# Performance work log

Measured on AMD Instinct MI355X. Metric: run time of the kernel, lower is better.

Reference implementation:

```python
import jax, jax.numpy as jnp
import numpy as np

NUM_MAPS = 512
NUM_BLOCKS = 2
ZG = 512
HID = min(96, NUM_MAPS)          # shared query / attention hidden dim
SEQ = 8                           # hardcoded inner sequence length
H1 = min(NUM_MAPS // 32, 3)       # num_heads1 = 3
H2 = NUM_MAPS // 32               # num_heads2 = 16
NPROC = NUM_BLOCKS * 4            # 4 FiLM param types per block


def _mha(q, k, v, nheads):
    """Multi-head attention. q:(Lq,D) k,v:(Lk,D) -> (Lq,D)."""
    Lq, D = q.shape
    Lk = k.shape[0]
    d = D // nheads
    qh = q.reshape(Lq, nheads, d).transpose(1, 0, 2)   # (h,Lq,d)
    kh = k.reshape(Lk, nheads, d).transpose(1, 0, 2)
    vh = v.reshape(Lk, nheads, d).transpose(1, 0, 2)
    A = jax.nn.softmax(jnp.einsum('hqd,hkd->hqk', qh, kh) / jnp.sqrt(jnp.asarray(D, q.dtype)))
    O = jnp.einsum('hqk,hkd->hqd', A, vh)
    return O.transpose(1, 0, 2).reshape(Lq, D)


def setup_inputs() -> dict:
    key = jax.random.key(0)
    ks = jax.random.split(key, 20)
    s = 0.05
    n = jax.random.normal
    return {
        'gate': jax.random.uniform(ks[0], (1, SEQ), dtype=jnp.float32),
        'x': n(ks[1], (1, ZG), dtype=jnp.float32),
        # shared_layer_alphaC : Linear(ZG, NUM_MAPS) + Sigmoid
        'Wa': n(ks[2], (ZG, NUM_MAPS)) * s, 'ba': jnp.zeros((NUM_MAPS,)),
        # shared_layer_Query : Linear(ZG, HID) + ReLU
        'Wqr': n(ks[3], (ZG, HID)) * s, 'bqr': jnp.zeros((HID,)),
        # stacked FiLM params: [block, {g1,b1,g2,b2}, num_maps, 8]
        'P': n(ks[4], (NUM_BLOCKS, 4, NUM_MAPS, SEQ)) * 0.2,
        'De': n(ks[5], (NUM_BLOCKS, 4, NUM_MAPS, SEQ)) * 0.01,
        'regs': n(ks[6], (NUM_BLOCKS, 4, NUM_MAPS)) * 0.001,
        # SMAB_small processor weights, stacked over the 8 processors
        'Wq1': n(ks[7], (NPROC, NUM_MAPS, HID)) * s,
        'Wk1': n(ks[8], (NPROC, NUM_MAPS, HID)) * s,
        'Wv1': n(ks[9], (NPROC, NUM_MAPS, HID)) * s,
        'fc1': n(ks[10], (NPROC, HID, HID)) * s,
        'Wq2': n(ks[11], (NPROC, HID, HID)) * s,
        'Wk2': n(ks[12], (NPROC, HID, HID)) * s,
        'Wv2': n(ks[13], (NPROC, HID, HID)) * s,
        'fc2': n(ks[14], (NPROC, HID, HID)) * s,
        'Wo': n(ks[15], (NPROC, HID, NUM_MAPS)) * s,
    }


def reference(gate, x, Wa, ba, Wqr, bqr, P, De, regs,
              Wq1, Wk1, Wv1, fc1, Wq2, Wk2, Wv2, fc2, Wo):
    alpha = jax.nn.sigmoid(x @ Wa + ba).reshape(-1)        # (NUM_MAPS,)
    q = jax.nn.relu(x @ Wqr + bqr)                          # (1, HID)

    # per-processor key/value set: transpose(1,0).view(1,8,num_maps)
    K_all = P.reshape(NPROC, NUM_MAPS, SEQ).transpose(0, 2, 1)  # (8procs, 8, NUM_MAPS)

    def smab(K, wq1, wk1, wv1, f1, wq2, wk2, wv2, f2, wo):
        # stage 1: self-attention over the 8-element set (num_heads1)
        Qk = K @ wq1                                        # (8, HID)
        H = Qk + _mha(Qk, K @ wk1, K @ wv1, H1)
        H = H + jax.nn.relu(H @ f1)
        # stage 2: task query attends to the set (num_heads2)
        Qq = q @ wq2                                        # (1, HID)
        O = Qq + _mha(Qq, H @ wk2, H @ wv2, H2)
        O = O + jax.nn.relu(O @ f2)
        return (O @ wo)[0]                                  # (NUM_MAPS,)

    trans = jax.vmap(smab)(K_all, Wq1, Wk1, Wv1, fc1, Wq2, Wk2, Wv2, fc2, Wo)
    trans = trans.reshape(NUM_BLOCKS, 4, NUM_MAPS)

    de = (De * gate[0]).sum(-1)                             # (NB,4,NUM_MAPS)
    mix = alpha * trans + (1.0 - alpha) * de
    offs = jnp.array([1.0, 0.0, 1.0, 0.0], dtype=mix.dtype).reshape(1, 4, 1)
    # gamma gets +1 offset, beta does not
    return mix * regs + offs
```

## Files before the change

kernel.cpp:

```cpp
#include <hip/hip_runtime.h>
#include <hip/hip_bf16.h>
#include <math.h>


#define WS_ALPHA 0
#define WS_Q     512
#define WS_QKV   608
#define WS_H     19040
#define WS_QQ    25184
#define WS_H2    25952
#define WS_K2    32096
#define WS_V2    38240
#define WS_OF    44384

__global__ __launch_bounds__(256) void k1_qkv_alpha_q(
    const float* __restrict__ x, const float* __restrict__ Wa,
    const float* __restrict__ ba, const float* __restrict__ Wqr,
    const float* __restrict__ bqr, const float* __restrict__ P,
    const float* __restrict__ Wq1, const float* __restrict__ Wk1,
    const float* __restrict__ Wv1, float* __restrict__ ws)
{
    __shared__ float sK[8 * 512];
    __shared__ float sp[256];
    const int blk = blockIdx.x, tid = threadIdx.x;

    if (blk < 576) {
        const int proc = blk / 72, c = blk % 72;
        const float4* P4 = (const float4*)(P + proc * 4096);
        for (int i = tid; i < 1024; i += 256) {
            float4 v = P4[i];
            const int m = i >> 1, off = (i & 1) * 4;
            sK[(off + 0) * 512 + m] = v.x;
            sK[(off + 1) * 512 + m] = v.y;
            sK[(off + 2) * 512 + m] = v.z;
            sK[(off + 3) * 512 + m] = v.w;
        }
        __syncthreads();
        const int rl = tid & 31, sp8 = tid >> 5;
        const int r = c * 32 + rl;
        const int mat = r / 768, r2 = r % 768;
        const int s = r2 / 96, h = r2 % 96;
        const float* W = (mat == 0 ? Wq1 : (mat == 1 ? Wk1 : Wv1))
                         + proc * 49152 + (sp8 * 64) * 96 + h;
        const float* Ks = sK + s * 512 + sp8 * 64;
        float acc = 0.f;
        #pragma unroll
        for (int m2 = 0; m2 < 64; ++m2) acc += Ks[m2] * W[m2 * 96];
        sp[tid] = acc;
        __syncthreads();
        if (sp8 == 0) {
            float a = 0.f;
            #pragma unroll
            for (int j = 0; j < 8; ++j) a += sp[rl + 32 * j];
            ws[WS_QKV + proc * 2304 + r] = a;
        }
    } else if (blk < 592) {
        for (int k = tid; k < 512; k += 256) sK[k] = x[k];
        __syncthreads();
        const int ml = tid & 31, sp8 = tid >> 5;
        const int m = (blk - 576) * 32 + ml;
        const float* W = Wa + (sp8 * 64) * 512 + m;
        const float* xq = sK + sp8 * 64;
        float acc = 0.f;
        #pragma unroll
        for (int k = 0; k < 64; ++k) acc += xq[k] * W[k * 512];
        sp[tid] = acc;
        __syncthreads();
        if (sp8 == 0) {
            float a = ba[m];
            #pragma unroll
            for (int j = 0; j < 8; ++j) a += sp[ml + 32 * j];
            ws[WS_ALPHA + m] = 1.f / (1.f + __expf(-a));
        }
    } else {
        for (int k = tid; k < 512; k += 256) sK[k] = x[k];
        __syncthreads();
        const int hl = tid & 31, sp8 = tid >> 5;
        const int h = (blk - 592) * 32 + hl;
        const float* W = Wqr + (sp8 * 64) * 96 + h;
        const float* xq = sK + sp8 * 64;
        float acc = 0.f;
        #pragma unroll
        for (int k = 0; k < 64; ++k) acc += xq[k] * W[k * 96];
        sp[tid] = acc;
        __syncthreads();
        if (sp8 == 0) {
            float a = bqr[h];
            #pragma unroll
            for (int j = 0; j < 8; ++j) a += sp[hl + 32 * j];
            ws[WS_Q + h] = fmaxf(a, 0.f);
        }
    }
}

__global__ __launch_bounds__(256) void k2a_attn1_qq(
    const float* __restrict__ Wq2, float* __restrict__ ws)
{
    const int blk = blockIdx.x, tid = threadIdx.x;
    const float rs = 0.10206207261596577f;

    if (blk < 8) {
        const int proc = blk;
        __shared__ float sQk[768], sKk[768], sVv[768], sH[768], sS[192];
        const float* qkv = ws + WS_QKV + proc * 2304;
        for (int i = tid; i < 768; i += 256) {
            sQk[i] = qkv[i]; sKk[i] = qkv[768 + i]; sVv[i] = qkv[1536 + i];
        }
        __syncthreads();
        if (tid < 192) {
            const int h0 = tid / 64, rem = tid % 64, si = rem / 8, sk = rem % 8;
            float acc = 0.f;
            #pragma unroll
            for (int d = 0; d < 32; ++d)
                acc += sQk[si * 96 + h0 * 32 + d] * sKk[sk * 96 + h0 * 32 + d];
            sS[tid] = acc * rs;
        }
        __syncthreads();
        if (tid < 24) {
            const int h0 = tid / 8, si = tid % 8;
            const float* row = sS + h0 * 64 + si * 8;
            float mx = row[0];
            #pragma unroll
            for (int k = 1; k < 8; ++k) mx = fmaxf(mx, row[k]);
            float e[8], sum = 0.f;
            #pragma unroll
            for (int k = 0; k < 8; ++k) { e[k] = __expf(row[k] - mx); sum += e[k]; }
            const float inv = 1.f / sum;
            #pragma unroll
            for (int d = 0; d < 32; ++d) {
                float o = 0.f;
                #pragma unroll
                for (int k = 0; k < 8; ++k) o += e[k] * sVv[k * 96 + h0 * 32 + d];
                const int idx = si * 96 + h0 * 32 + d;
                sH[idx] = sQk[idx] + o * inv;
            }
        }
        __syncthreads();
        float* Hout = ws + WS_H + proc * 768;
        for (int i = tid; i < 768; i += 256) Hout[i] = sH[i];
    } else {
        const int b2 = blk - 8, proc = b2 / 3, t = b2 % 3;
        __shared__ float sq[96], sp[256];
        if (tid < 96) sq[tid] = ws[WS_Q + tid];
        __syncthreads();
        const int jl = tid & 31, ks = tid >> 5;
        const int j = 32 * t + jl;
        const float* W = Wq2 + proc * 9216 + j;
        float acc = 0.f;
        #pragma unroll
        for (int i = 0; i < 12; ++i)
            acc += sq[12 * ks + i] * W[(12 * ks + i) * 96];
        sp[tid] = acc;
        __syncthreads();
        if (ks == 0) {
            float a = 0.f;
            #pragma unroll
            for (int u = 0; u < 8; ++u) a += sp[jl + 32 * u];
            ws[WS_QQ + proc * 96 + j] = a;
        }
    }
}

__global__ __launch_bounds__(256) void k2b_fc1(
    const float* __restrict__ fc1, float* __restrict__ ws)
{
    const int b = blockIdx.x, proc = b / 3, t = b % 3, tid = threadIdx.x;
    __shared__ float sH[768];
    const float* Hin = ws + WS_H + proc * 768;
    for (int i = tid; i < 768; i += 256) sH[i] = Hin[i];
    __syncthreads();
    const int s = tid >> 5, jl = tid & 31, j = 32 * t + jl;
    const float* W = fc1 + proc * 9216 + j;
    const float* Hs = sH + s * 96;
    float acc = 0.f;
    #pragma unroll
    for (int i = 0; i < 96; ++i) acc += Hs[i] * W[i * 96];
    ws[WS_H2 + proc * 768 + s * 96 + j] = Hs[j] + fmaxf(acc, 0.f);
}

__global__ __launch_bounds__(256) void k2c_kv2(
    const float* __restrict__ Wk2, const float* __restrict__ Wv2,
    float* __restrict__ ws)
{
    const int b = blockIdx.x, proc = b / 6, rem = b % 6;
    const int mat = rem / 3, t = rem % 3, tid = threadIdx.x;
    __shared__ float sH[768];
    const float* Hin = ws + WS_H2 + proc * 768;
    for (int i = tid; i < 768; i += 256) sH[i] = Hin[i];
    __syncthreads();
    const int s = tid >> 5, jl = tid & 31, j = 32 * t + jl;
    const float* W = (mat ? Wv2 : Wk2) + proc * 9216 + j;
    const float* Hs = sH + s * 96;
    float acc = 0.f;
    #pragma unroll
    for (int i = 0; i < 96; ++i) acc += Hs[i] * W[i * 96];
    ws[(mat ? WS_V2 : WS_K2) + proc * 768 + s * 96 + j] = acc;
}

__global__ __launch_bounds__(256) void k2d_attn2_fc2(
    const float* __restrict__ fc2, float* __restrict__ ws)
{
    const int b = blockIdx.x, proc = b / 3, t = b % 3, tid = threadIdx.x;
    __shared__ float sK2[768], sV2[768], sQq[96], sO[96], sp[256];
    const float rs = 0.10206207261596577f;
    for (int i = tid; i < 768; i += 256) {
        sK2[i] = ws[WS_K2 + proc * 768 + i];
        sV2[i] = ws[WS_V2 + proc * 768 + i];
    }
    if (tid < 96) sQq[tid] = ws[WS_QQ + proc * 96 + tid];
    __syncthreads();
    if (tid < 16) {
        const int h0 = tid;
        float lg[8], mx = -1e30f;
        #pragma unroll
        for (int k = 0; k < 8; ++k) {
            float acc = 0.f;
            #pragma unroll
            for (int d = 0; d < 6; ++d)
                acc += sQq[h0 * 6 + d] * sK2[k * 96 + h0 * 6 + d];
            lg[k] = acc * rs; mx = fmaxf(mx, lg[k]);
        }
        float e[8], sum = 0.f;
        #pragma unroll
        for (int k = 0; k < 8; ++k) { e[k] = __expf(lg[k] - mx); sum += e[k]; }
        const float inv = 1.f / sum;
        #pragma unroll
        for (int d = 0; d < 6; ++d) {
            float o = 0.f;
            #pragma unroll
            for (int k = 0; k < 8; ++k) o += e[k] * sV2[k * 96 + h0 * 6 + d];
            sO[h0 * 6 + d] = sQq[h0 * 6 + d] + o * inv;
        }
    }
    __syncthreads();
    const int jl = tid & 31, ks = tid >> 5;
    const int j = 32 * t + jl;
    const float* W = fc2 + proc * 9216 + j;
    float acc = 0.f;
    #pragma unroll
    for (int i = 0; i < 12; ++i)
        acc += sO[12 * ks + i] * W[(12 * ks + i) * 96];
    sp[tid] = acc;
    __syncthreads();
    if (ks == 0) {
        float a = 0.f;
        #pragma unroll
        for (int u = 0; u < 8; ++u) a += sp[jl + 32 * u];
        ws[WS_OF + proc * 96 + j] = sO[j] + fmaxf(a, 0.f);
    }
}

__global__ __launch_bounds__(256) void k2e_out(
    const float* __restrict__ gate, const float* __restrict__ De,
    const float* __restrict__ regs, const float* __restrict__ Wo,
    const float* __restrict__ ws, float* __restrict__ out)
{
    const int b = blockIdx.x, proc = b >> 3, e = b & 7, tid = threadIdx.x;
    __shared__ float sOf[96], sg[8], sp[256];
    if (tid < 96) sOf[tid] = ws[WS_OF + proc * 96 + tid];
    else if (tid < 104) sg[tid - 96] = gate[tid - 96];
    __syncthreads();
    const int ml = tid & 63, ks = tid >> 6;
    const int m = 64 * e + ml;
    const float* W = Wo + proc * 49152 + m;
    float acc = 0.f;
    #pragma unroll
    for (int i = 0; i < 24; ++i)
        acc += sOf[24 * ks + i] * W[(24 * ks + i) * 512];
    sp[tid] = acc;
    __syncthreads();
    if (ks == 0) {
        const float tr = sp[ml] + sp[ml + 64] + sp[ml + 128] + sp[ml + 192];
        const float4* Dp4 = (const float4*)(De + proc * 4096 + m * 8);
        const float4 d0 = Dp4[0], d1 = Dp4[1];
        const float de = d0.x * sg[0] + d0.y * sg[1] + d0.z * sg[2] + d0.w * sg[3]
                       + d1.x * sg[4] + d1.y * sg[5] + d1.z * sg[6] + d1.w * sg[7];
        const float a = ws[WS_ALPHA + m];
        const float mix = a * tr + (1.f - a) * de;
        const int pt = proc & 3;
        const float off = (pt == 0 || pt == 2) ? 1.f : 0.f;
        out[proc * 512 + m] = mix * regs[proc * 512 + m] + off;
    }
}

extern "C" void kernel_launch(void* const* d_in, const int* in_sizes, int n_in,
                              void* d_out, int out_size, void* d_ws, size_t ws_size,
                              hipStream_t stream)
{
    const float* gate = (const float*)d_in[0];
    const float* x    = (const float*)d_in[1];
    const float* Wa   = (const float*)d_in[2];
    const float* ba   = (const float*)d_in[3];
    const float* Wqr  = (const float*)d_in[4];
    const float* bqr  = (const float*)d_in[5];
    const float* P    = (const float*)d_in[6];
    const float* De   = (const float*)d_in[7];
    const float* regs = (const float*)d_in[8];
    const float* Wq1  = (const float*)d_in[9];
    const float* Wk1  = (const float*)d_in[10];
    const float* Wv1  = (const float*)d_in[11];
    const float* fc1  = (const float*)d_in[12];
    const float* Wq2  = (const float*)d_in[13];
    const float* Wk2  = (const float*)d_in[14];
    const float* Wv2  = (const float*)d_in[15];
    const float* fc2  = (const float*)d_in[16];
    const float* Wo   = (const float*)d_in[17];
    float* ws = (float*)d_ws;

    hipLaunchKernelGGL(k1_qkv_alpha_q, dim3(595), dim3(256), 0, stream,
                       x, Wa, ba, Wqr, bqr, P, Wq1, Wk1, Wv1, ws);
    hipLaunchKernelGGL(k2a_attn1_qq, dim3(32), dim3(256), 0, stream, Wq2, ws);
    hipLaunchKernelGGL(k2b_fc1, dim3(24), dim3(256), 0, stream, fc1, ws);
    hipLaunchKernelGGL(k2c_kv2, dim3(48), dim3(256), 0, stream, Wk2, Wv2, ws);
    hipLaunchKernelGGL(k2d_attn2_fc2, dim3(24), dim3(256), 0, stream, fc2, ws);
    hipLaunchKernelGGL(k2e_out, dim3(64), dim3(256), 0, stream,
                       gate, De, regs, Wo, ws, (float*)d_out);
}
```

Baseline: 115.9 us.

## Fuse six launches into three and restructure the QKV projection for reuse

Merges attention-1, fc1 and the K2/V2 projections into one kernel, and Qq, attention-2, fc2 and the output projection into another, so three launches are removed. Each fused block recomputes the small per-processor work (attn1, fc1, Qq, fc2) redundantly instead of round-tripping through the workspace. The QKV kernel is regridded so each thread reuses one weight load across all 8 sequence rows, using padded shared memory to avoid bank conflicts, which cuts blocks from 595 to 179. The cost is duplicated compute per block and fewer blocks to spread across the GPU.

```diff
diff --git a/kernel.cpp b/kernel.cpp
--- a/kernel.cpp
+++ b/kernel.cpp
@@ -6,209 +6,201 @@
 #define WS_ALPHA 0
 #define WS_Q     512
 #define WS_QKV   608
-#define WS_H     19040
-#define WS_QQ    25184
-#define WS_H2    25952
-#define WS_K2    32096
-#define WS_V2    38240
-#define WS_OF    44384
-
-__global__ __launch_bounds__(256) void k1_qkv_alpha_q(
+#define WS_K2    19040
+#define WS_V2    25184
+
+__global__ __launch_bounds__(256) void kA_qkv_alpha_q(
     const float* __restrict__ x, const float* __restrict__ Wa,
     const float* __restrict__ ba, const float* __restrict__ Wqr,
     const float* __restrict__ bqr, const float* __restrict__ P,
     const float* __restrict__ Wq1, const float* __restrict__ Wk1,
     const float* __restrict__ Wv1, float* __restrict__ ws)
 {
-    __shared__ float sK[8 * 512];
-    __shared__ float sp[256];
+    __shared__ float sK[8 * 528];
+    __shared__ float sp[2048];
     const int blk = blockIdx.x, tid = threadIdx.x;
 
-    if (blk < 576) {
-        const int proc = blk / 72, c = blk % 72;
+    if (blk < 144) {
+        const int proc = blk / 18, rem = blk % 18, mat = rem / 6, six = rem % 6;
         const float4* P4 = (const float4*)(P + proc * 4096);
         for (int i = tid; i < 1024; i += 256) {
             float4 v = P4[i];
-            const int m = i >> 1, off = (i & 1) * 4;
-            sK[(off + 0) * 512 + m] = v.x;
-            sK[(off + 1) * 512 + m] = v.y;
-            sK[(off + 2) * 512 + m] = v.z;
-            sK[(off + 3) * 512 + m] = v.w;
-        }
-        __syncthreads();
-        const int rl = tid & 31, sp8 = tid >> 5;
-        const int r = c * 32 + rl;
-        const int mat = r / 768, r2 = r % 768;
-        const int s = r2 / 96, h = r2 % 96;
+            const int c = i >> 1, off = (i & 1) * 4;
+            const int cp = c + (c >> 5);
+            sK[(off + 0) * 528 + cp] = v.x;
+            sK[(off + 1) * 528 + cp] = v.y;
+            sK[(off + 2) * 528 + cp] = v.z;
+            sK[(off + 3) * 528 + cp] = v.w;
+        }
+        __syncthreads();
+        const int hl = tid & 15, ks = tid >> 4;
+        const int h = six * 16 + hl;
         const float* W = (mat == 0 ? Wq1 : (mat == 1 ? Wk1 : Wv1))
-                         + proc * 49152 + (sp8 * 64) * 96 + h;
-        const float* Ks = sK + s * 512 + sp8 * 64;
-        float acc = 0.f;
-        #pragma unroll
-        for (int m2 = 0; m2 < 64; ++m2) acc += Ks[m2] * W[m2 * 96];
-        sp[tid] = acc;
-        __syncthreads();
-        if (sp8 == 0) {
+                         + proc * 49152 + (ks * 32) * 96 + h;
+        const float* Kb = sK + ks * 33;
+        float acc[8] = {0.f,0.f,0.f,0.f,0.f,0.f,0.f,0.f};
+        #pragma unroll
+        for (int m2 = 0; m2 < 32; ++m2) {
+            const float w = W[m2 * 96];
+            const float* Kc = Kb + m2;
+            #pragma unroll
+            for (int s = 0; s < 8; ++s) acc[s] += Kc[s * 528] * w;
+        }
+        float* spb = sp + ks * 128 + hl * 8;
+        #pragma unroll
+        for (int s = 0; s < 8; ++s) spb[s] = acc[s];
+        __syncthreads();
+        if (tid < 128) {
             float a = 0.f;
             #pragma unroll
-            for (int j = 0; j < 8; ++j) a += sp[rl + 32 * j];
-            ws[WS_QKV + proc * 2304 + r] = a;
-        }
-    } else if (blk < 592) {
+            for (int u = 0; u < 16; ++u) a += sp[u * 128 + tid];
+            const int hl2 = tid >> 3, s = tid & 7;
+            ws[WS_QKV + proc * 2304 + mat * 768 + s * 96 + six * 16 + hl2] = a;
+        }
+    } else if (blk < 176) {
         for (int k = tid; k < 512; k += 256) sK[k] = x[k];
         __syncthreads();
-        const int ml = tid & 31, sp8 = tid >> 5;
-        const int m = (blk - 576) * 32 + ml;
-        const float* W = Wa + (sp8 * 64) * 512 + m;
-        const float* xq = sK + sp8 * 64;
-        float acc = 0.f;
-        #pragma unroll
-        for (int k = 0; k < 64; ++k) acc += xq[k] * W[k * 512];
-        sp[tid] = acc;
-        __syncthreads();
-        if (sp8 == 0) {
-            float a = ba[m];
-            #pragma unroll
-            for (int j = 0; j < 8; ++j) a += sp[ml + 32 * j];
-            ws[WS_ALPHA + m] = 1.f / (1.f + __expf(-a));
+        const int ml = tid & 15, ks = tid >> 4;
+        const int m = (blk - 144) * 16 + ml;
+        const float* W = Wa + (ks * 32) * 512 + m;
+        const float* xq = sK + ks * 32;
+        float acc = 0.f;
+        #pragma unroll
+        for (int k = 0; k < 32; ++k) acc += xq[k] * W[k * 512];
+        sp[tid] = acc;
+        __syncthreads();
+        if (tid < 16) {
+            float a = ba[(blk - 144) * 16 + tid];
+            #pragma unroll
+            for (int u = 0; u < 16; ++u) a += sp[u * 16 + tid];
+            ws[WS_ALPHA + (blk - 144) * 16 + tid] = 1.f / (1.f + __expf(-a));
         }
     } else {
         for (int k = tid; k < 512; k += 256) sK[k] = x[k];
         __syncthreads();
-        const int hl = tid & 31, sp8 = tid >> 5;
-        const int h = (blk - 592) * 32 + hl;
-        const float* W = Wqr + (sp8 * 64) * 96 + h;
-        const float* xq = sK + sp8 * 64;
+        const int hl = tid & 31, ks = tid >> 5;
+        const int h = (blk - 176) * 32 + hl;
+        const float* W = Wqr + (ks * 64) * 96 + h;
+        const float* xq = sK + ks * 64;
         float acc = 0.f;
         #pragma unroll
         for (int k = 0; k < 64; ++k) acc += xq[k] * W[k * 96];
         sp[tid] = acc;
         __syncthreads();
-        if (sp8 == 0) {
+        if (ks == 0) {
             float a = bqr[h];
             #pragma unroll
-            for (int j = 0; j < 8; ++j) a += sp[hl + 32 * j];
+            for (int u = 0; u < 8; ++u) a += sp[hl + 32 * u];
             ws[WS_Q + h] = fmaxf(a, 0.f);
         }
     }
 }
 
-__global__ __launch_bounds__(256) void k2a_attn1_qq(
-    const float* __restrict__ Wq2, float* __restrict__ ws)
-{
-    const int blk = blockIdx.x, tid = threadIdx.x;
-    const float rs = 0.10206207261596577f;
-
-    if (blk < 8) {
-        const int proc = blk;
-        __shared__ float sQk[768], sKk[768], sVv[768], sH[768], sS[192];
-        const float* qkv = ws + WS_QKV + proc * 2304;
-        for (int i = tid; i < 768; i += 256) {
-            sQk[i] = qkv[i]; sKk[i] = qkv[768 + i]; sVv[i] = qkv[1536 + i];
-        }
-        __syncthreads();
-        if (tid < 192) {
-            const int h0 = tid / 64, rem = tid % 64, si = rem / 8, sk = rem % 8;
-            float acc = 0.f;
-            #pragma unroll
-            for (int d = 0; d < 32; ++d)
-                acc += sQk[si * 96 + h0 * 32 + d] * sKk[sk * 96 + h0 * 32 + d];
-            sS[tid] = acc * rs;
-        }
-        __syncthreads();
-        if (tid < 24) {
-            const int h0 = tid / 8, si = tid % 8;
-            const float* row = sS + h0 * 64 + si * 8;
-            float mx = row[0];
-            #pragma unroll
-            for (int k = 1; k < 8; ++k) mx = fmaxf(mx, row[k]);
-            float e[8], sum = 0.f;
-            #pragma unroll
-            for (int k = 0; k < 8; ++k) { e[k] = __expf(row[k] - mx); sum += e[k]; }
-            const float inv = 1.f / sum;
-            #pragma unroll
-            for (int d = 0; d < 32; ++d) {
-                float o = 0.f;
-                #pragma unroll
-                for (int k = 0; k < 8; ++k) o += e[k] * sVv[k * 96 + h0 * 32 + d];
-                const int idx = si * 96 + h0 * 32 + d;
-                sH[idx] = sQk[idx] + o * inv;
-            }
-        }
-        __syncthreads();
-        float* Hout = ws + WS_H + proc * 768;
-        for (int i = tid; i < 768; i += 256) Hout[i] = sH[i];
-    } else {
-        const int b2 = blk - 8, proc = b2 / 3, t = b2 % 3;
-        __shared__ float sq[96], sp[256];
-        if (tid < 96) sq[tid] = ws[WS_Q + tid];
-        __syncthreads();
-        const int jl = tid & 31, ks = tid >> 5;
-        const int j = 32 * t + jl;
-        const float* W = Wq2 + proc * 9216 + j;
-        float acc = 0.f;
-        #pragma unroll
-        for (int i = 0; i < 12; ++i)
-            acc += sq[12 * ks + i] * W[(12 * ks + i) * 96];
-        sp[tid] = acc;
-        __syncthreads();
-        if (ks == 0) {
-            float a = 0.f;
-            #pragma unroll
-            for (int u = 0; u < 8; ++u) a += sp[jl + 32 * u];
-            ws[WS_QQ + proc * 96 + j] = a;
-        }
-    }
-}
-
-__global__ __launch_bounds__(256) void k2b_fc1(
-    const float* __restrict__ fc1, float* __restrict__ ws)
-{
-    const int b = blockIdx.x, proc = b / 3, t = b % 3, tid = threadIdx.x;
-    __shared__ float sH[768];
-    const float* Hin = ws + WS_H + proc * 768;
-    for (int i = tid; i < 768; i += 256) sH[i] = Hin[i];
-    __syncthreads();
-    const int s = tid >> 5, jl = tid & 31, j = 32 * t + jl;
-    const float* W = fc1 + proc * 9216 + j;
-    const float* Hs = sH + s * 96;
-    float acc = 0.f;
-    #pragma unroll
-    for (int i = 0; i < 96; ++i) acc += Hs[i] * W[i * 96];
-    ws[WS_H2 + proc * 768 + s * 96 + j] = Hs[j] + fmaxf(acc, 0.f);
-}
-
-__global__ __launch_bounds__(256) void k2c_kv2(
-    const float* __restrict__ Wk2, const float* __restrict__ Wv2,
-    float* __restrict__ ws)
+__global__ __launch_bounds__(256) void kB_attn1_fc1_kv2(
+    const float* __restrict__ fc1w, const float* __restrict__ Wk2,
+    const float* __restrict__ Wv2, float* __restrict__ ws)
 {
     const int b = blockIdx.x, proc = b / 6, rem = b % 6;
     const int mat = rem / 3, t = rem % 3, tid = threadIdx.x;
-    __shared__ float sH[768];
-    const float* Hin = ws + WS_H2 + proc * 768;
-    for (int i = tid; i < 768; i += 256) sH[i] = Hin[i];
-    __syncthreads();
-    const int s = tid >> 5, jl = tid & 31, j = 32 * t + jl;
+    __shared__ float sQk[768], sKk[768], sVv[768], sH[768], sH2[768], sS[192];
+    const float rs = 0.10206207261596577f;
+
+    const float* qkv = ws + WS_QKV + proc * 2304;
+    for (int i = tid; i < 768; i += 256) {
+        sQk[i] = qkv[i]; sKk[i] = qkv[768 + i]; sVv[i] = qkv[1536 + i];
+    }
+    __syncthreads();
+    if (tid < 192) {
+        const int h0 = tid / 64, r64 = tid % 64, si = r64 / 8, sk = r64 % 8;
+        float acc = 0.f;
+        #pragma unroll
+        for (int d = 0; d < 32; ++d)
+            acc += sQk[si * 96 + h0 * 32 + d] * sKk[sk * 96 + h0 * 32 + d];
+        sS[tid] = acc * rs;
+    }
+    __syncthreads();
+    if (tid < 24) {
+        float* row = sS + tid * 8;
+        float mx = row[0];
+        #pragma unroll
+        for (int k = 1; k < 8; ++k) mx = fmaxf(mx, row[k]);
+        float e[8], sum = 0.f;
+        #pragma unroll
+        for (int k = 0; k < 8; ++k) { e[k] = __expf(row[k] - mx); sum += e[k]; }
+        const float inv = 1.f / sum;
+        #pragma unroll
+        for (int k = 0; k < 8; ++k) row[k] = e[k] * inv;
+    }
+    __syncthreads();
+    if (tid < 192) {
+        const int h0 = tid / 64, r64 = tid % 64, si = r64 / 8, dq = r64 % 8;
+        const float* e = sS + h0 * 64 + si * 8;
+        float o0 = 0.f, o1 = 0.f, o2 = 0.f, o3 = 0.f;
+        #pragma unroll
+        for (int k = 0; k < 8; ++k) {
+            const float ek = e[k];
+            const float* v = sVv + k * 96 + h0 * 32 + dq * 4;
+            o0 += ek * v[0]; o1 += ek * v[1]; o2 += ek * v[2]; o3 += ek * v[3];
+        }
+        const int base = si * 96 + h0 * 32 + dq * 4;
+        sH[base + 0] = sQk[base + 0] + o0;
+        sH[base + 1] = sQk[base + 1] + o1;
+        sH[base + 2] = sQk[base + 2] + o2;
+        sH[base + 3] = sQk[base + 3] + o3;
+    }
+    __syncthreads();
+    #pragma unroll
+    for (int r = 0; r < 3; ++r) {
+        const int idx = tid + 256 * r, s = idx / 96, j = idx % 96;
+        const float* W = fc1w + proc * 9216 + j;
+        const float* Hs = sH + s * 96;
+        float acc = 0.f;
+        #pragma unroll
+        for (int i = 0; i < 96; ++i) acc += Hs[i] * W[i * 96];
+        sH2[idx] = sH[idx] + fmaxf(acc, 0.f);
+    }
+    __syncthreads();
+    const int s = tid >> 5, jl = tid & 31, j = t * 32 + jl;
     const float* W = (mat ? Wv2 : Wk2) + proc * 9216 + j;
-    const float* Hs = sH + s * 96;
+    const float* Hs = sH2 + s * 96;
     float acc = 0.f;
     #pragma unroll
     for (int i = 0; i < 96; ++i) acc += Hs[i] * W[i * 96];
     ws[(mat ? WS_V2 : WS_K2) + proc * 768 + s * 96 + j] = acc;
 }
 
-__global__ __launch_bounds__(256) void k2d_attn2_fc2(
-    const float* __restrict__ fc2, float* __restrict__ ws)
-{
-    const int b = blockIdx.x, proc = b / 3, t = b % 3, tid = threadIdx.x;
-    __shared__ float sK2[768], sV2[768], sQq[96], sO[96], sp[256];
+__global__ __launch_bounds__(256) void kC_qq_attn2_fc2_out(
+    const float* __restrict__ gate, const float* __restrict__ De,
+    const float* __restrict__ regs, const float* __restrict__ Wq2,
+    const float* __restrict__ fc2w, const float* __restrict__ Wo,
+    const float* __restrict__ ws, float* __restrict__ out)
+{
+    const int b = blockIdx.x, proc = b >> 3, e = b & 7, tid = threadIdx.x;
+    __shared__ float sK2[768], sV2[768];
+    __shared__ float sq[96], sQq[96], sO[96], sOf[96], sE2[128], sg[8], sp[256];
     const float rs = 0.10206207261596577f;
+
     for (int i = tid; i < 768; i += 256) {
         sK2[i] = ws[WS_K2 + proc * 768 + i];
         sV2[i] = ws[WS_V2 + proc * 768 + i];
     }
-    if (tid < 96) sQq[tid] = ws[WS_QQ + proc * 96 + tid];
-    __syncthreads();
+    if (tid < 96) sq[tid] = ws[WS_Q + tid];
+    else if (tid >= 96 && tid < 104) sg[tid - 96] = gate[tid - 96];
+    __syncthreads();
+
+    if (tid < 192) {
+        const int j = tid % 96, ks = tid / 96;
+        const float* W = Wq2 + proc * 9216 + j + (ks * 48) * 96;
+        const float* xq = sq + ks * 48;
+        float acc = 0.f;
+        #pragma unroll
+        for (int i = 0; i < 48; ++i) acc += xq[i] * W[i * 96];
+        sp[tid] = acc;
+    }
+    __syncthreads();
+    if (tid < 96) sQq[tid] = sp[tid] + sp[96 + tid];
+    __syncthreads();
+
     if (tid < 16) {
         const int h0 = tid;
         float lg[8], mx = -1e30f;
@@ -220,46 +212,35 @@
                 acc += sQq[h0 * 6 + d] * sK2[k * 96 + h0 * 6 + d];
             lg[k] = acc * rs; mx = fmaxf(mx, lg[k]);
         }
-        float e[8], sum = 0.f;
-        #pragma unroll
-        for (int k = 0; k < 8; ++k) { e[k] = __expf(lg[k] - mx); sum += e[k]; }
+        float ex[8], sum = 0.f;
+        #pragma unroll
+        for (int k = 0; k < 8; ++k) { ex[k] = __expf(lg[k] - mx); sum += ex[k]; }
         const float inv = 1.f / sum;
         #pragma unroll
-        for (int d = 0; d < 6; ++d) {
-            float o = 0.f;
-            #pragma unroll
-            for (int k = 0; k < 8; ++k) o += e[k] * sV2[k * 96 + h0 * 6 + d];
-            sO[h0 * 6 + d] = sQq[h0 * 6 + d] + o * inv;
-        }
-    }
-    __syncthreads();
-    const int jl = tid & 31, ks = tid >> 5;
-    const int j = 32 * t + jl;
-    const float* W = fc2 + proc * 9216 + j;
-    float acc = 0.f;
-    #pragma unroll
-    for (int i = 0; i < 12; ++i)
-        acc += sO[12 * ks + i] * W[(12 * ks + i) * 96];
-    sp[tid] = acc;
-    __syncthreads();
-    if (ks == 0) {
-        float a = 0.f;
-        #pragma unroll
-        for (int u = 0; u < 8; ++u) a += sp[jl + 32 * u];
-        ws[WS_OF + proc * 96 + j] = sO[j] + fmaxf(a, 0.f);
-    }
-}
-
-__global__ __launch_bounds__(256) void k2e_out(
-    const float* __restrict__ gate, const float* __restrict__ De,
-    const float* __restrict__ regs, const float* __restrict__ Wo,
-    const float* __restrict__ ws, float* __restrict__ out)
-{
-    const int b = blockIdx.x, proc = b >> 3, e = b & 7, tid = threadIdx.x;
-    __shared__ float sOf[96], sg[8], sp[256];
-    if (tid < 96) sOf[tid] = ws[WS_OF + proc * 96 + tid];
-    else if (tid < 104) sg[tid - 96] = gate[tid - 96];
-    __syncthreads();
+        for (int k = 0; k < 8; ++k) sE2[h0 * 8 + k] = ex[k] * inv;
+    }
+    __syncthreads();
+    if (tid < 96) {
+        const int h0 = tid / 6;
+        float o = 0.f;
+        #pragma unroll
+        for (int k = 0; k < 8; ++k) o += sE2[h0 * 8 + k] * sV2[k * 96 + tid];
+        sO[tid] = sQq[tid] + o;
+    }
+    __syncthreads();
+    if (tid < 192) {
+        const int j = tid % 96, ks = tid / 96;
+        const float* W = fc2w + proc * 9216 + j + (ks * 48) * 96;
+        const float* Os = sO + ks * 48;
+        float acc = 0.f;
+        #pragma unroll
+        for (int i = 0; i < 48; ++i) acc += Os[i] * W[i * 96];
+        sp[tid] = acc;
+    }
+    __syncthreads();
+    if (tid < 96) sOf[tid] = sO[tid] + fmaxf(sp[tid] + sp[96 + tid], 0.f);
+    __syncthreads();
+
     const int ml = tid & 63, ks = tid >> 6;
     const int m = 64 * e + ml;
     const float* W = Wo + proc * 49152 + m;
@@ -307,12 +288,10 @@
     const float* Wo   = (const float*)d_in[17];
     float* ws = (float*)d_ws;
 
-    hipLaunchKernelGGL(k1_qkv_alpha_q, dim3(595), dim3(256), 0, stream,
+    hipLaunchKernelGGL(kA_qkv_alpha_q, dim3(179), dim3(256), 0, stream,
                        x, Wa, ba, Wqr, bqr, P, Wq1, Wk1, Wv1, ws);
-    hipLaunchKernelGGL(k2a_attn1_qq, dim3(32), dim3(256), 0, stream, Wq2, ws);
-    hipLaunchKernelGGL(k2b_fc1, dim3(24), dim3(256), 0, stream, fc1, ws);
-    hipLaunchKernelGGL(k2c_kv2, dim3(48), dim3(256), 0, stream, Wk2, Wv2, ws);
-    hipLaunchKernelGGL(k2d_attn2_fc2, dim3(24), dim3(256), 0, stream, fc2, ws);
-    hipLaunchKernelGGL(k2e_out, dim3(64), dim3(256), 0, stream,
-                       gate, De, regs, Wo, ws, (float*)d_out);
-}
+    hipLaunchKernelGGL(kB_attn1_fc1_kv2, dim3(48), dim3(256), 0, stream,
+                       fc1, Wk2, Wv2, ws);
+    hipLaunchKernelGGL(kC_qq_attn2_fc2_out, dim3(64), dim3(256), 0, stream,
+                       gate, De, regs, Wq2, fc2, Wo, ws, (float*)d_out);
+}
```

Result: faster. 109.8 us (-5.3%).
